# Kernel optimization log

Hardware: AMD Instinct MI355X
Metric: run time of the kernel (lower is better)

Reference implementation:

```python
import jax, jax.numpy as jnp
import numpy as np

N_NODES = 50000
N_EDGES = 800000
F_IN, F_HID, F_OUT = 128, 64, 32


def setup_inputs() -> dict:
    key = jax.random.key(0)
    k1, k2, k3, k4, k5, k6 = jax.random.split(key, 6)
    x = jax.random.normal(k1, (N_NODES, F_IN), dtype=jnp.float32)
    edge_index = jax.random.randint(k2, (2, N_EDGES), 0, N_NODES, dtype=jnp.int64)
    # Glorot-ish init for the two GCNConv linear layers
    W1 = jax.random.normal(k3, (F_IN, F_HID), dtype=jnp.float32) / np.sqrt(F_IN)
    b1 = jnp.zeros((F_HID,), dtype=jnp.float32)
    W2 = jax.random.normal(k4, (F_HID, F_OUT), dtype=jnp.float32) / np.sqrt(F_HID)
    b2 = jnp.zeros((F_OUT,), dtype=jnp.float32)
    return {"x": x, "edge_index": edge_index, "W1": W1, "b1": b1, "W2": W2, "b2": b2}


def _gcn_conv(x, src, dst, norm, W, b):
    # GCNConv: linear transform, then D^{-1/2}(A+I)D^{-1/2} aggregation
    xw = x @ W                                # [N, F_out]
    msg = xw[src] * norm[:, None]             # [E+N, F_out] gather + scale
    out = jax.ops.segment_sum(msg, dst, num_segments=x.shape[0])
    return out + b


def reference(x, edge_index, W1, b1, W2, b2):
    n = x.shape[0]
    self_loops = jnp.arange(n, dtype=edge_index.dtype)
    src = jnp.concatenate([edge_index[0], self_loops])  # [E+N]
    dst = jnp.concatenate([edge_index[1], self_loops])
    # symmetric degree normalization (self-loops guarantee deg >= 1)
    deg = jax.ops.segment_sum(jnp.ones_like(dst, dtype=x.dtype), dst, num_segments=n)
    dinv = jax.lax.rsqrt(deg)
    norm = dinv[src] * dinv[dst]              # [E+N]

    h = _gcn_conv(x, src, dst, norm, W1, b1)
    h = jax.nn.relu(h)
    # dropout p=0.5 is identity in eval mode (training=False)
    out = _gcn_conv(h, src, dst, norm, W2, b2)
    return out
```

## Files before the change

kernel.cpp:

```cpp
#include <hip/hip_runtime.h>
#include <hip/hip_fp16.h>

#define NN 50000
#define NE 800000
#define F_IN 128
#define F_HID 64
#define F_OUT 32
#define CAP 48
#define NBUCK 196
#define EPB 4096
#define CELL 64
#define NXW1 782

typedef _Float16 f16x8 __attribute__((ext_vector_type(8)));
typedef float f32x4 __attribute__((ext_vector_type(4)));
#define XS_STR 136


__global__ __launch_bounds__(256) void fused_xw1_partition_kernel(
        const float* __restrict__ x, const float* __restrict__ W,
        const int* __restrict__ src, const int* __restrict__ dst,
        int* __restrict__ cnt2t, unsigned int* __restrict__ bstore2,
        __half* __restrict__ outh) {
    __shared__ _Float16 xs[64 * XS_STR];
    __shared__ _Float16 wt[64 * XS_STR];
    __shared__ int hist[4][NBUCK];
    __shared__ int cur[NBUCK];
    int t = threadIdx.x;

    if (blockIdx.x < NBUCK) {
        int blk = blockIdx.x;
        for (int i = t; i < 4 * NBUCK; i += 256) ((int*)hist)[i] = 0;
        __syncthreads();
        int wv = t >> 6;
        int base = blk * EPB;
        unsigned int pk[16];
#pragma unroll
        for (int i = 0; i < 16; ++i) {
            int e = base + i * 256 + t;
            if (e < NE) {
                unsigned int d = (unsigned int)dst[e];
                unsigned int s = (unsigned int)src[e];
                pk[i] = (d << 16) | s;
                atomicAdd(&hist[wv][d >> 8], 1);
            } else {
                pk[i] = 0xFFFFFFFFu;
            }
        }
        __syncthreads();
        for (int b = t; b < NBUCK; b += 256) {
            int h = hist[0][b] + hist[1][b] + hist[2][b] + hist[3][b];
            cur[b] = 0;
            cnt2t[b * NBUCK + blk] = h;
        }
        __syncthreads();
#pragma unroll
        for (int i = 0; i < 16; ++i) {
            unsigned int p = pk[i];
            if (p != 0xFFFFFFFFu) {
                int b = p >> 24;
                int pos = atomicAdd(&cur[b], 1);
                if (pos < CELL) bstore2[((size_t)blk * NBUCK + b) * CELL + pos] = p;
            }
        }
        return;
    }

    int node0 = (blockIdx.x - NBUCK) * 64;

    {
        int r = t >> 2;
        int c0 = (t & 3) * 32;
        int gn = node0 + r;
        if (gn > NN - 1) gn = NN - 1;
        const float4* xrow = (const float4*)(x + (size_t)gn * F_IN);
#pragma unroll
        for (int i = 0; i < 8; ++i) {
            float4 v = xrow[(c0 >> 2) + i];
            _Float16* p = &xs[r * XS_STR + c0 + i * 4];
            p[0] = (_Float16)v.x; p[1] = (_Float16)v.y;
            p[2] = (_Float16)v.z; p[3] = (_Float16)v.w;
        }
    }
#pragma unroll
    for (int i = 0; i < 8; ++i) {
        int idx4 = t + i * 256;
        int k = idx4 >> 4;
        int n0 = (idx4 & 15) << 2;
        float4 v = ((const float4*)W)[idx4];
        wt[(n0 + 0) * XS_STR + k] = (_Float16)v.x;
        wt[(n0 + 1) * XS_STR + k] = (_Float16)v.y;
        wt[(n0 + 2) * XS_STR + k] = (_Float16)v.z;
        wt[(n0 + 3) * XS_STR + k] = (_Float16)v.w;
    }
    __syncthreads();

    int wave = t >> 6;
    int l = t & 63;
    int quad = l >> 4;
    int lm = l & 15;

    f32x4 acc[4] = {{0,0,0,0},{0,0,0,0},{0,0,0,0},{0,0,0,0}};
    const _Float16* abase = &xs[(wave * 16 + lm) * XS_STR + quad * 8];
#pragma unroll
    for (int kk4 = 0; kk4 < 4; ++kk4) {
        int kk = kk4 * 32;
        f16x8 a = *(const f16x8*)(abase + kk);
#pragma unroll
        for (int ft = 0; ft < 4; ++ft) {
            f16x8 b = *(const f16x8*)&wt[(ft * 16 + lm) * XS_STR + kk + quad * 8];
            acc[ft] = __builtin_amdgcn_mfma_f32_16x16x32_f16(a, b, acc[ft], 0, 0, 0);
        }
    }

    __syncthreads();
    _Float16* ot = xs;
#pragma unroll
    for (int ft = 0; ft < 4; ++ft) {
#pragma unroll
        for (int r = 0; r < 4; ++r) {
            int row_l = wave * 16 + quad * 4 + r;
            ot[row_l * 64 + ft * 16 + lm] = (_Float16)acc[ft][r];
        }
    }
    __syncthreads();
#pragma unroll
    for (int i = 0; i < 2; ++i) {
        int idx = t + i * 256;
        int row = idx >> 3;
        int c8 = (idx & 7) * 8;
        int gn = node0 + row;
        if (gn < NN)
            *(uint4*)(outh + (size_t)gn * 64 + c8) = *(const uint4*)&ot[row * 64 + c8];
    }
}


__device__ __forceinline__ void slot_insert(unsigned int p, int* cnt_l,
                                            unsigned short* slot_l) {
    int dl = (p >> 16) & 255;
    int pos = atomicAdd(&cnt_l[dl], 1);
    if (pos < CAP) slot_l[dl * CAP + pos] = (unsigned short)(p & 0xFFFFu);
}

__global__ __launch_bounds__(256) void build_slots_kernel(
        const int* __restrict__ cnt2t, const unsigned int* __restrict__ bstore2,
        unsigned short* __restrict__ slot, int* __restrict__ cnt_g, float* __restrict__ dinv) {
    __shared__ unsigned short slot_l[256 * CAP];
    __shared__ int cnt_l[256];
    int t = threadIdx.x;
    int b = blockIdx.x;
    cnt_l[t] = 0;
    __syncthreads();

    for (int blk = t; blk < NBUCK; blk += 256) {
        int c = cnt2t[b * NBUCK + blk];
        if (c > CELL) c = CELL;
        const unsigned int* seg = bstore2 + ((size_t)blk * NBUCK + b) * CELL;
        int j = 0;
        for (; j + 4 <= c; j += 4) {
            unsigned int p0 = seg[j + 0];
            unsigned int p1 = seg[j + 1];
            unsigned int p2 = seg[j + 2];
            unsigned int p3 = seg[j + 3];
            slot_insert(p0, cnt_l, slot_l);
            slot_insert(p1, cnt_l, slot_l);
            slot_insert(p2, cnt_l, slot_l);
            slot_insert(p3, cnt_l, slot_l);
        }
        for (; j < c; ++j) slot_insert(seg[j], cnt_l, slot_l);
    }
    __syncthreads();

    unsigned int* sg = (unsigned int*)(slot + (size_t)b * 256 * CAP);
    const unsigned int* sl = (const unsigned int*)slot_l;
    for (int j = t; j < 256 * CAP / 2; j += 256) sg[j] = sl[j];

    int n = b * 256 + t;
    if (n < NN) {
        int c = cnt_l[t];
        cnt_g[n] = c;
        dinv[n] = rsqrtf(1.0f + (float)c);
    }
}


__global__ __launch_bounds__(256, 4) void gather64_w2_kernel(
        const __half* __restrict__ xw, const int* __restrict__ cnt,
        const unsigned short* __restrict__ slot, const float* __restrict__ dinv,
        const float* __restrict__ b1, const float* __restrict__ W2,
        __half* __restrict__ hw2h) {
    __shared__ float w2s[F_HID * F_OUT];
    __shared__ float hl[4][F_HID];
    int t = threadIdx.x;
    for (int i = t; i < F_HID * F_OUT / 4; i += 256)
        ((float4*)w2s)[i] = ((const float4*)W2)[i];
    __syncthreads();

    int lane = t & 63;
    int wv = t >> 6;
    int n = blockIdx.x * 4 + wv;
    int st = lane >> 4;
    int fl4 = lane & 15;
    const uint2* base = (const uint2*)xw;
    int deg = cnt[n];
    if (deg > CAP) deg = CAP;
    float din = dinv[n];
    const unsigned short* srow = slot + (size_t)n * CAP;
    float a0 = 0, a1 = 0, a2 = 0, a3 = 0;
    int e = st;
    for (; e + 12 < deg; e += 16) {
        int s0 = srow[e];
        int s1 = srow[e + 4];
        int s2 = srow[e + 8];
        int s3 = srow[e + 12];
        float dv0 = dinv[s0], dv1 = dinv[s1], dv2 = dinv[s2], dv3 = dinv[s3];
        uint2 u0 = base[(size_t)s0 * 16 + fl4];
        uint2 u1 = base[(size_t)s1 * 16 + fl4];
        uint2 u2 = base[(size_t)s2 * 16 + fl4];
        uint2 u3 = base[(size_t)s3 * 16 + fl4];
        float2 p0 = __half22float2(*(__half2*)&u0.x), p1 = __half22float2(*(__half2*)&u0.y);
        float2 q0 = __half22float2(*(__half2*)&u1.x), q1 = __half22float2(*(__half2*)&u1.y);
        float2 r0 = __half22float2(*(__half2*)&u2.x), r1 = __half22float2(*(__half2*)&u2.y);
        float2 t0 = __half22float2(*(__half2*)&u3.x), t1 = __half22float2(*(__half2*)&u3.y);
        a0 += dv0 * p0.x + dv1 * q0.x + dv2 * r0.x + dv3 * t0.x;
        a1 += dv0 * p0.y + dv1 * q0.y + dv2 * r0.y + dv3 * t0.y;
        a2 += dv0 * p1.x + dv1 * q1.x + dv2 * r1.x + dv3 * t1.x;
        a3 += dv0 * p1.y + dv1 * q1.y + dv2 * r1.y + dv3 * t1.y;
    }
    for (; e < deg; e += 4) {
        int s = srow[e];
        float dv = dinv[s];
        uint2 u = base[(size_t)s * 16 + fl4];
        float2 p0 = __half22float2(*(__half2*)&u.x);
        float2 p1 = __half22float2(*(__half2*)&u.y);
        a0 += dv * p0.x; a1 += dv * p0.y; a2 += dv * p1.x; a3 += dv * p1.y;
    }
    a0 += __shfl_xor(a0, 16, 64); a1 += __shfl_xor(a1, 16, 64);
    a2 += __shfl_xor(a2, 16, 64); a3 += __shfl_xor(a3, 16, 64);
    a0 += __shfl_xor(a0, 32, 64); a1 += __shfl_xor(a1, 32, 64);
    a2 += __shfl_xor(a2, 32, 64); a3 += __shfl_xor(a3, 32, 64);
    if (st == 0) {
        uint2 u = base[(size_t)n * 16 + fl4];
        float2 s0 = __half22float2(*(__half2*)&u.x);
        float2 s1 = __half22float2(*(__half2*)&u.y);
        float4 bb = ((const float4*)b1)[fl4];
        float v0 = din * (a0 + din * s0.x) + bb.x;
        float v1 = din * (a1 + din * s0.y) + bb.y;
        float v2 = din * (a2 + din * s1.x) + bb.z;
        float v3 = din * (a3 + din * s1.y) + bb.w;
        float* hr = &hl[wv][fl4 * 4];
        hr[0] = v0 > 0.f ? v0 : 0.f;
        hr[1] = v1 > 0.f ? v1 : 0.f;
        hr[2] = v2 > 0.f ? v2 : 0.f;
        hr[3] = v3 > 0.f ? v3 : 0.f;
    }
    asm volatile("s_waitcnt lgkmcnt(0)" ::: "memory");
    {
        int f = lane & 31;
        int kh = lane >> 5;
        const float* hr = &hl[wv][kh * 32];
        float acc = 0.0f;
#pragma unroll
        for (int k = 0; k < 32; ++k) acc += hr[k] * w2s[(kh * 32 + k) * F_OUT + f];
        acc += __shfl_xor(acc, 32, 64);
        if (kh == 0) hw2h[(size_t)n * F_OUT + f] = __float2half(acc * din);
    }
}


__global__ __launch_bounds__(256, 8) void gather32_kernel(
        const __half* __restrict__ scaled, const int* __restrict__ cnt,
        const unsigned short* __restrict__ slot, const float* __restrict__ dinv,
        const float* __restrict__ bias, float* __restrict__ out) {
    int lane = threadIdx.x & 63;
    int n = blockIdx.x * 4 + (threadIdx.x >> 6);
    if (n >= NN) return;
    int st = lane >> 3;
    int fl4 = lane & 7;
    const uint2* base = (const uint2*)scaled;
    int deg = cnt[n];
    if (deg > CAP) deg = CAP;
    const unsigned short* srow = slot + (size_t)n * CAP;
    float a0 = 0, a1 = 0, a2 = 0, a3 = 0;
    int e = st;
    for (; e + 8 < deg; e += 16) {
        int s0 = srow[e];
        int s1 = srow[e + 8];
        uint2 u0 = base[(size_t)s0 * 8 + fl4];
        uint2 u1 = base[(size_t)s1 * 8 + fl4];
        float2 p0 = __half22float2(*(__half2*)&u0.x);
        float2 p1 = __half22float2(*(__half2*)&u0.y);
        float2 q0 = __half22float2(*(__half2*)&u1.x);
        float2 q1 = __half22float2(*(__half2*)&u1.y);
        a0 += p0.x + q0.x; a1 += p0.y + q0.y;
        a2 += p1.x + q1.x; a3 += p1.y + q1.y;
    }
    for (; e < deg; e += 8) {
        int s = srow[e];
        uint2 u = base[(size_t)s * 8 + fl4];
        float2 p0 = __half22float2(*(__half2*)&u.x);
        float2 p1 = __half22float2(*(__half2*)&u.y);
        a0 += p0.x; a1 += p0.y; a2 += p1.x; a3 += p1.y;
    }
    a0 += __shfl_xor(a0, 8, 64);  a1 += __shfl_xor(a1, 8, 64);
    a2 += __shfl_xor(a2, 8, 64);  a3 += __shfl_xor(a3, 8, 64);
    a0 += __shfl_xor(a0, 16, 64); a1 += __shfl_xor(a1, 16, 64);
    a2 += __shfl_xor(a2, 16, 64); a3 += __shfl_xor(a3, 16, 64);
    a0 += __shfl_xor(a0, 32, 64); a1 += __shfl_xor(a1, 32, 64);
    a2 += __shfl_xor(a2, 32, 64); a3 += __shfl_xor(a3, 32, 64);
    if (st == 0) {
        uint2 u = base[(size_t)n * 8 + fl4];
        float2 s0 = __half22float2(*(__half2*)&u.x);
        float2 s1 = __half22float2(*(__half2*)&u.y);
        float4 b4 = ((const float4*)bias)[fl4];
        float di = dinv[n];
        float4 r;
        r.x = di * (a0 + s0.x) + b4.x;
        r.y = di * (a1 + s0.y) + b4.y;
        r.z = di * (a2 + s1.x) + b4.z;
        r.w = di * (a3 + s1.y) + b4.w;
        ((float4*)out)[(size_t)n * 8 + fl4] = r;
    }
}


extern "C" void kernel_launch(void* const* d_in, const int* in_sizes, int n_in,
                              void* d_out, int out_size, void* d_ws, size_t ws_size,
                              hipStream_t stream) {
    const float* x  = (const float*)d_in[0];
    const int*   ei = (const int*)d_in[1];
    const float* W1 = (const float*)d_in[2];
    const float* b1 = (const float*)d_in[3];
    const float* W2 = (const float*)d_in[4];
    const float* b2 = (const float*)d_in[5];
    const int* src = ei;
    const int* dst = ei + NE;

    float*          ws      = (float*)d_ws;
    float*          dinv    = ws;
    int*            cnt     = (int*)(ws + 50048);
    int*            cnt2t   = (int*)(ws + 100096);
    unsigned int*   bstore2 = (unsigned int*)(ws + 138624);
    unsigned short* slot    = (unsigned short*)(ws + 2597248);
    __half*         xw1h    = (__half*)(ws + 3801472);
    __half*         hw2h    = (__half*)(ws + 5401472);
    float*          out     = (float*)d_out;

    fused_xw1_partition_kernel<<<NBUCK + NXW1, 256, 0, stream>>>(
        x, W1, src, dst, cnt2t, bstore2, xw1h);
    build_slots_kernel<<<NBUCK, 256, 0, stream>>>(cnt2t, bstore2, slot, cnt, dinv);
    gather64_w2_kernel<<<NN / 4, 256, 0, stream>>>(xw1h, cnt, slot, dinv, b1, W2, hw2h);
    gather32_kernel<<<NN / 4, 256, 0, stream>>>(hw2h, cnt, slot, dinv, b2, out);
}
```

Measured before the change: 150.6 us.

## Merge four kernels into one persistent kernel with software grid barriers

Replaces the four separate launches (partition plus XW1, slot build, layer-1 gather with W2, layer-2 gather) with a single persistent kernel. It is sized to the occupancy-limited resident grid, loops over work units, and separates phases with atomic-counter grid barriers. The aim is to remove per-launch overhead and inter-kernel gaps. In exchange it adds system-scope fences and spin-waits at each barrier, a memset and host-side property queries on every call. The grid is also capped at 1024 blocks and limited by the shared union LDS, which may reduce parallelism in the gather phases.

Result: slower. 515.9 us (+242.6%).

```diff
diff --git a/kernel.cpp b/kernel.cpp
--- a/kernel.cpp
+++ b/kernel.cpp
@@ -11,316 +11,323 @@
 #define EPB 4096
 #define CELL 64
 #define NXW1 782
+#define NGRP 12500
 
 typedef _Float16 f16x8 __attribute__((ext_vector_type(8)));
 typedef float f32x4 __attribute__((ext_vector_type(4)));
 #define XS_STR 136
 
-
-__global__ __launch_bounds__(256) void fused_xw1_partition_kernel(
-        const float* __restrict__ x, const float* __restrict__ W,
+__device__ __forceinline__ void grid_barrier(int* bar, int phase, int G) {
+    __syncthreads();
+    if (threadIdx.x == 0) {
+        __threadfence_system();
+        int ticket = __hip_atomic_fetch_add(&bar[0], 1, __ATOMIC_ACQ_REL,
+                                            __HIP_MEMORY_SCOPE_SYSTEM);
+        if (ticket == phase * G - 1) {
+            __threadfence_system();
+            __hip_atomic_store(&bar[1], phase, __ATOMIC_RELEASE,
+                               __HIP_MEMORY_SCOPE_SYSTEM);
+        } else {
+            while (__hip_atomic_load(&bar[1], __ATOMIC_ACQUIRE,
+                                     __HIP_MEMORY_SCOPE_SYSTEM) < phase)
+                __builtin_amdgcn_s_sleep(8);
+        }
+        __threadfence_system();
+    }
+    __syncthreads();
+}
+
+__global__ __launch_bounds__(256, 4) void mega_kernel(
+        const float* __restrict__ x, const float* __restrict__ W1,
+        const float* __restrict__ b1, const float* __restrict__ W2,
+        const float* __restrict__ b2,
         const int* __restrict__ src, const int* __restrict__ dst,
         int* __restrict__ cnt2t, unsigned int* __restrict__ bstore2,
-        __half* __restrict__ outh) {
-    __shared__ _Float16 xs[64 * XS_STR];
-    __shared__ _Float16 wt[64 * XS_STR];
-    __shared__ int hist[4][NBUCK];
-    __shared__ int cur[NBUCK];
+        unsigned short* __restrict__ slot, int* __restrict__ cnt_g,
+        float* __restrict__ dinv, __half* __restrict__ xw1h,
+        __half* __restrict__ hw2h, float* __restrict__ out, int* bar) {
+    __shared__ __align__(16) char lds[34816];
     int t = threadIdx.x;
-
-    if (blockIdx.x < NBUCK) {
-        int blk = blockIdx.x;
-        for (int i = t; i < 4 * NBUCK; i += 256) ((int*)hist)[i] = 0;
-        __syncthreads();
+    int G = gridDim.x;
+
+    for (int u = blockIdx.x; u < NBUCK + NXW1; u += G) {
+        __syncthreads();
+        if (u < NBUCK) {
+            int blk = u;
+            int (*hist)[NBUCK] = (int(*)[NBUCK])lds;
+            int* cur = (int*)(lds + 3136);
+            for (int i = t; i < 4 * NBUCK; i += 256) ((int*)hist)[i] = 0;
+            __syncthreads();
+            int wv = t >> 6;
+            int base = blk * EPB;
+            unsigned int pk[16];
+#pragma unroll
+            for (int i = 0; i < 16; ++i) {
+                int e = base + i * 256 + t;
+                if (e < NE) {
+                    unsigned int d = (unsigned int)dst[e];
+                    unsigned int s = (unsigned int)src[e];
+                    pk[i] = (d << 16) | s;
+                    atomicAdd(&hist[wv][d >> 8], 1);
+                } else pk[i] = 0xFFFFFFFFu;
+            }
+            __syncthreads();
+            for (int b = t; b < NBUCK; b += 256) {
+                cur[b] = 0;
+                cnt2t[b * NBUCK + blk] = hist[0][b] + hist[1][b] + hist[2][b] + hist[3][b];
+            }
+            __syncthreads();
+#pragma unroll
+            for (int i = 0; i < 16; ++i) {
+                unsigned int p = pk[i];
+                if (p != 0xFFFFFFFFu) {
+                    int b = p >> 24;
+                    int pos = atomicAdd(&cur[b], 1);
+                    if (pos < CELL) bstore2[((size_t)blk * NBUCK + b) * CELL + pos] = p;
+                }
+            }
+        } else {
+            int node0 = (u - NBUCK) * 64;
+            _Float16* xs = (_Float16*)lds;
+            _Float16* wt = xs + 64 * XS_STR;
+            {
+                int r = t >> 2;
+                int c0 = (t & 3) * 32;
+                int gn = node0 + r;
+                if (gn > NN - 1) gn = NN - 1;
+                const float4* xrow = (const float4*)(x + (size_t)gn * F_IN);
+#pragma unroll
+                for (int i = 0; i < 8; ++i) {
+                    float4 v = xrow[(c0 >> 2) + i];
+                    _Float16* p = &xs[r * XS_STR + c0 + i * 4];
+                    p[0] = (_Float16)v.x; p[1] = (_Float16)v.y;
+                    p[2] = (_Float16)v.z; p[3] = (_Float16)v.w;
+                }
+            }
+#pragma unroll
+            for (int i = 0; i < 8; ++i) {
+                int idx4 = t + i * 256;
+                int k = idx4 >> 4;
+                int n0 = (idx4 & 15) << 2;
+                float4 v = ((const float4*)W1)[idx4];
+                wt[(n0 + 0) * XS_STR + k] = (_Float16)v.x;
+                wt[(n0 + 1) * XS_STR + k] = (_Float16)v.y;
+                wt[(n0 + 2) * XS_STR + k] = (_Float16)v.z;
+                wt[(n0 + 3) * XS_STR + k] = (_Float16)v.w;
+            }
+            __syncthreads();
+            int wave = t >> 6;
+            int l = t & 63;
+            int quad = l >> 4;
+            int lm = l & 15;
+            f32x4 acc[4] = {{0,0,0,0},{0,0,0,0},{0,0,0,0},{0,0,0,0}};
+            const _Float16* abase = &xs[(wave * 16 + lm) * XS_STR + quad * 8];
+#pragma unroll
+            for (int kk4 = 0; kk4 < 4; ++kk4) {
+                int kk = kk4 * 32;
+                f16x8 a = *(const f16x8*)(abase + kk);
+#pragma unroll
+                for (int ft = 0; ft < 4; ++ft) {
+                    f16x8 b = *(const f16x8*)&wt[(ft * 16 + lm) * XS_STR + kk + quad * 8];
+                    acc[ft] = __builtin_amdgcn_mfma_f32_16x16x32_f16(a, b, acc[ft], 0, 0, 0);
+                }
+            }
+            __syncthreads();
+            _Float16* ot = xs;
+#pragma unroll
+            for (int ft = 0; ft < 4; ++ft) {
+#pragma unroll
+                for (int r = 0; r < 4; ++r) {
+                    int row_l = wave * 16 + quad * 4 + r;
+                    ot[row_l * 64 + ft * 16 + lm] = (_Float16)acc[ft][r];
+                }
+            }
+            __syncthreads();
+#pragma unroll
+            for (int i = 0; i < 2; ++i) {
+                int idx = t + i * 256;
+                int row = idx >> 3;
+                int c8 = (idx & 7) * 8;
+                int gn = node0 + row;
+                if (gn < NN)
+                    *(uint4*)(xw1h + (size_t)gn * 64 + c8) = *(const uint4*)&ot[row * 64 + c8];
+            }
+        }
+    }
+    grid_barrier(bar, 1, G);
+
+    for (int b = blockIdx.x; b < NBUCK; b += G) {
+        unsigned short* slot_l = (unsigned short*)lds;
+        int* cnt_l = (int*)(lds + 24576);
+        cnt_l[t] = 0;
+        __syncthreads();
+        for (int blk = t; blk < NBUCK; blk += 256) {
+            int c = cnt2t[b * NBUCK + blk];
+            if (c > CELL) c = CELL;
+            const unsigned int* seg = bstore2 + ((size_t)blk * NBUCK + b) * CELL;
+            int j = 0;
+            for (; j + 4 <= c; j += 4) {
+                unsigned int p0 = seg[j + 0];
+                unsigned int p1 = seg[j + 1];
+                unsigned int p2 = seg[j + 2];
+                unsigned int p3 = seg[j + 3];
+#pragma unroll
+                for (int q = 0; q < 4; ++q) {
+                    unsigned int p = (q == 0) ? p0 : (q == 1) ? p1 : (q == 2) ? p2 : p3;
+                    int dl = (p >> 16) & 255;
+                    int pos = atomicAdd(&cnt_l[dl], 1);
+                    if (pos < CAP) slot_l[dl * CAP + pos] = (unsigned short)(p & 0xFFFFu);
+                }
+            }
+            for (; j < c; ++j) {
+                unsigned int p = seg[j];
+                int dl = (p >> 16) & 255;
+                int pos = atomicAdd(&cnt_l[dl], 1);
+                if (pos < CAP) slot_l[dl * CAP + pos] = (unsigned short)(p & 0xFFFFu);
+            }
+        }
+        __syncthreads();
+        unsigned int* sg = (unsigned int*)(slot + (size_t)b * 256 * CAP);
+        const unsigned int* sl = (const unsigned int*)slot_l;
+        for (int j = t; j < 256 * CAP / 2; j += 256) sg[j] = sl[j];
+        int n = b * 256 + t;
+        if (n < NN) {
+            int c = cnt_l[t];
+            cnt_g[n] = c;
+            dinv[n] = rsqrtf(1.0f + (float)c);
+        }
+        __syncthreads();
+    }
+    grid_barrier(bar, 2, G);
+
+    {
+        float* w2s = (float*)lds;
+        float (*hl)[F_HID] = (float(*)[F_HID])(lds + 8192);
+        for (int i = t; i < F_HID * F_OUT / 4; i += 256)
+            ((float4*)w2s)[i] = ((const float4*)W2)[i];
+        __syncthreads();
+        int lane = t & 63;
         int wv = t >> 6;
-        int base = blk * EPB;
-        unsigned int pk[16];
-#pragma unroll
-        for (int i = 0; i < 16; ++i) {
-            int e = base + i * 256 + t;
-            if (e < NE) {
-                unsigned int d = (unsigned int)dst[e];
-                unsigned int s = (unsigned int)src[e];
-                pk[i] = (d << 16) | s;
-                atomicAdd(&hist[wv][d >> 8], 1);
-            } else {
-                pk[i] = 0xFFFFFFFFu;
-            }
-        }
-        __syncthreads();
-        for (int b = t; b < NBUCK; b += 256) {
-            int h = hist[0][b] + hist[1][b] + hist[2][b] + hist[3][b];
-            cur[b] = 0;
-            cnt2t[b * NBUCK + blk] = h;
-        }
-        __syncthreads();
-#pragma unroll
-        for (int i = 0; i < 16; ++i) {
-            unsigned int p = pk[i];
-            if (p != 0xFFFFFFFFu) {
-                int b = p >> 24;
-                int pos = atomicAdd(&cur[b], 1);
-                if (pos < CELL) bstore2[((size_t)blk * NBUCK + b) * CELL + pos] = p;
-            }
-        }
-        return;
-    }
-
-    int node0 = (blockIdx.x - NBUCK) * 64;
+        int st = lane >> 4;
+        int fl4 = lane & 15;
+        const uint2* base = (const uint2*)xw1h;
+        for (int g = blockIdx.x; g < NGRP; g += G) {
+            int n = g * 4 + wv;
+            int deg = cnt_g[n];
+            if (deg > CAP) deg = CAP;
+            float din = dinv[n];
+            const unsigned short* srow = slot + (size_t)n * CAP;
+            float a0 = 0, a1 = 0, a2 = 0, a3 = 0;
+            int e = st;
+            for (; e + 12 < deg; e += 16) {
+                int s0 = srow[e], s1 = srow[e + 4], s2 = srow[e + 8], s3 = srow[e + 12];
+                float dv0 = dinv[s0], dv1 = dinv[s1], dv2 = dinv[s2], dv3 = dinv[s3];
+                uint2 u0 = base[(size_t)s0 * 16 + fl4];
+                uint2 u1 = base[(size_t)s1 * 16 + fl4];
+                uint2 u2 = base[(size_t)s2 * 16 + fl4];
+                uint2 u3 = base[(size_t)s3 * 16 + fl4];
+                float2 p0 = __half22float2(*(__half2*)&u0.x), p1 = __half22float2(*(__half2*)&u0.y);
+                float2 q0 = __half22float2(*(__half2*)&u1.x), q1 = __half22float2(*(__half2*)&u1.y);
+                float2 r0 = __half22float2(*(__half2*)&u2.x), r1 = __half22float2(*(__half2*)&u2.y);
+                float2 t0 = __half22float2(*(__half2*)&u3.x), t1 = __half22float2(*(__half2*)&u3.y);
+                a0 += dv0 * p0.x + dv1 * q0.x + dv2 * r0.x + dv3 * t0.x;
+                a1 += dv0 * p0.y + dv1 * q0.y + dv2 * r0.y + dv3 * t0.y;
+                a2 += dv0 * p1.x + dv1 * q1.x + dv2 * r1.x + dv3 * t1.x;
+                a3 += dv0 * p1.y + dv1 * q1.y + dv2 * r1.y + dv3 * t1.y;
+            }
+            for (; e < deg; e += 4) {
+                int s = srow[e];
+                float dv = dinv[s];
+                uint2 u = base[(size_t)s * 16 + fl4];
+                float2 p0 = __half22float2(*(__half2*)&u.x);
+                float2 p1 = __half22float2(*(__half2*)&u.y);
+                a0 += dv * p0.x; a1 += dv * p0.y; a2 += dv * p1.x; a3 += dv * p1.y;
+            }
+            a0 += __shfl_xor(a0, 16, 64); a1 += __shfl_xor(a1, 16, 64);
+            a2 += __shfl_xor(a2, 16, 64); a3 += __shfl_xor(a3, 16, 64);
+            a0 += __shfl_xor(a0, 32, 64); a1 += __shfl_xor(a1, 32, 64);
+            a2 += __shfl_xor(a2, 32, 64); a3 += __shfl_xor(a3, 32, 64);
+            if (st == 0) {
+                uint2 u = base[(size_t)n * 16 + fl4];
+                float2 s0 = __half22float2(*(__half2*)&u.x);
+                float2 s1 = __half22float2(*(__half2*)&u.y);
+                float4 bb = ((const float4*)b1)[fl4];
+                float v0 = din * (a0 + din * s0.x) + bb.x;
+                float v1 = din * (a1 + din * s0.y) + bb.y;
+                float v2 = din * (a2 + din * s1.x) + bb.z;
+                float v3 = din * (a3 + din * s1.y) + bb.w;
+                float* hr = &hl[wv][fl4 * 4];
+                hr[0] = v0 > 0.f ? v0 : 0.f;
+                hr[1] = v1 > 0.f ? v1 : 0.f;
+                hr[2] = v2 > 0.f ? v2 : 0.f;
+                hr[3] = v3 > 0.f ? v3 : 0.f;
+            }
+            asm volatile("s_waitcnt lgkmcnt(0)" ::: "memory");
+            {
+                int f = lane & 31;
+                int kh = lane >> 5;
+                const float* hr = &hl[wv][kh * 32];
+                float acc = 0.0f;
+#pragma unroll
+                for (int k = 0; k < 32; ++k) acc += hr[k] * w2s[(kh * 32 + k) * F_OUT + f];
+                acc += __shfl_xor(acc, 32, 64);
+                if (kh == 0) hw2h[(size_t)n * F_OUT + f] = __float2half(acc * din);
+            }
+        }
+    }
+    grid_barrier(bar, 3, G);
 
     {
-        int r = t >> 2;
-        int c0 = (t & 3) * 32;
-        int gn = node0 + r;
-        if (gn > NN - 1) gn = NN - 1;
-        const float4* xrow = (const float4*)(x + (size_t)gn * F_IN);
-#pragma unroll
-        for (int i = 0; i < 8; ++i) {
-            float4 v = xrow[(c0 >> 2) + i];
-            _Float16* p = &xs[r * XS_STR + c0 + i * 4];
-            p[0] = (_Float16)v.x; p[1] = (_Float16)v.y;
-            p[2] = (_Float16)v.z; p[3] = (_Float16)v.w;
-        }
-    }
-#pragma unroll
-    for (int i = 0; i < 8; ++i) {
-        int idx4 = t + i * 256;
-        int k = idx4 >> 4;
-        int n0 = (idx4 & 15) << 2;
-        float4 v = ((const float4*)W)[idx4];
-        wt[(n0 + 0) * XS_STR + k] = (_Float16)v.x;
-        wt[(n0 + 1) * XS_STR + k] = (_Float16)v.y;
-        wt[(n0 + 2) * XS_STR + k] = (_Float16)v.z;
-        wt[(n0 + 3) * XS_STR + k] = (_Float16)v.w;
-    }
-    __syncthreads();
-
-    int wave = t >> 6;
-    int l = t & 63;
-    int quad = l >> 4;
-    int lm = l & 15;
-
-    f32x4 acc[4] = {{0,0,0,0},{0,0,0,0},{0,0,0,0},{0,0,0,0}};
-    const _Float16* abase = &xs[(wave * 16 + lm) * XS_STR + quad * 8];
-#pragma unroll
-    for (int kk4 = 0; kk4 < 4; ++kk4) {
-        int kk = kk4 * 32;
-        f16x8 a = *(const f16x8*)(abase + kk);
-#pragma unroll
-        for (int ft = 0; ft < 4; ++ft) {
-            f16x8 b = *(const f16x8*)&wt[(ft * 16 + lm) * XS_STR + kk + quad * 8];
-            acc[ft] = __builtin_amdgcn_mfma_f32_16x16x32_f16(a, b, acc[ft], 0, 0, 0);
-        }
-    }
-
-    __syncthreads();
-    _Float16* ot = xs;
-#pragma unroll
-    for (int ft = 0; ft < 4; ++ft) {
-#pragma unroll
-        for (int r = 0; r < 4; ++r) {
-            int row_l = wave * 16 + quad * 4 + r;
-            ot[row_l * 64 + ft * 16 + lm] = (_Float16)acc[ft][r];
-        }
-    }
-    __syncthreads();
-#pragma unroll
-    for (int i = 0; i < 2; ++i) {
-        int idx = t + i * 256;
-        int row = idx >> 3;
-        int c8 = (idx & 7) * 8;
-        int gn = node0 + row;
-        if (gn < NN)
-            *(uint4*)(outh + (size_t)gn * 64 + c8) = *(const uint4*)&ot[row * 64 + c8];
-    }
-}
-
-
-__device__ __forceinline__ void slot_insert(unsigned int p, int* cnt_l,
-                                            unsigned short* slot_l) {
-    int dl = (p >> 16) & 255;
-    int pos = atomicAdd(&cnt_l[dl], 1);
-    if (pos < CAP) slot_l[dl * CAP + pos] = (unsigned short)(p & 0xFFFFu);
-}
-
-__global__ __launch_bounds__(256) void build_slots_kernel(
-        const int* __restrict__ cnt2t, const unsigned int* __restrict__ bstore2,
-        unsigned short* __restrict__ slot, int* __restrict__ cnt_g, float* __restrict__ dinv) {
-    __shared__ unsigned short slot_l[256 * CAP];
-    __shared__ int cnt_l[256];
-    int t = threadIdx.x;
-    int b = blockIdx.x;
-    cnt_l[t] = 0;
-    __syncthreads();
-
-    for (int blk = t; blk < NBUCK; blk += 256) {
-        int c = cnt2t[b * NBUCK + blk];
-        if (c > CELL) c = CELL;
-        const unsigned int* seg = bstore2 + ((size_t)blk * NBUCK + b) * CELL;
-        int j = 0;
-        for (; j + 4 <= c; j += 4) {
-            unsigned int p0 = seg[j + 0];
-            unsigned int p1 = seg[j + 1];
-            unsigned int p2 = seg[j + 2];
-            unsigned int p3 = seg[j + 3];
-            slot_insert(p0, cnt_l, slot_l);
-            slot_insert(p1, cnt_l, slot_l);
-            slot_insert(p2, cnt_l, slot_l);
-            slot_insert(p3, cnt_l, slot_l);
-        }
-        for (; j < c; ++j) slot_insert(seg[j], cnt_l, slot_l);
-    }
-    __syncthreads();
-
-    unsigned int* sg = (unsigned int*)(slot + (size_t)b * 256 * CAP);
-    const unsigned int* sl = (const unsigned int*)slot_l;
-    for (int j = t; j < 256 * CAP / 2; j += 256) sg[j] = sl[j];
-
-    int n = b * 256 + t;
-    if (n < NN) {
-        int c = cnt_l[t];
-        cnt_g[n] = c;
-        dinv[n] = rsqrtf(1.0f + (float)c);
-    }
-}
-
-
-__global__ __launch_bounds__(256, 4) void gather64_w2_kernel(
-        const __half* __restrict__ xw, const int* __restrict__ cnt,
-        const unsigned short* __restrict__ slot, const float* __restrict__ dinv,
-        const float* __restrict__ b1, const float* __restrict__ W2,
-        __half* __restrict__ hw2h) {
-    __shared__ float w2s[F_HID * F_OUT];
-    __shared__ float hl[4][F_HID];
-    int t = threadIdx.x;
-    for (int i = t; i < F_HID * F_OUT / 4; i += 256)
-        ((float4*)w2s)[i] = ((const float4*)W2)[i];
-    __syncthreads();
-
-    int lane = t & 63;
-    int wv = t >> 6;
-    int n = blockIdx.x * 4 + wv;
-    int st = lane >> 4;
-    int fl4 = lane & 15;
-    const uint2* base = (const uint2*)xw;
-    int deg = cnt[n];
-    if (deg > CAP) deg = CAP;
-    float din = dinv[n];
-    const unsigned short* srow = slot + (size_t)n * CAP;
-    float a0 = 0, a1 = 0, a2 = 0, a3 = 0;
-    int e = st;
-    for (; e + 12 < deg; e += 16) {
-        int s0 = srow[e];
-        int s1 = srow[e + 4];
-        int s2 = srow[e + 8];
-        int s3 = srow[e + 12];
-        float dv0 = dinv[s0], dv1 = dinv[s1], dv2 = dinv[s2], dv3 = dinv[s3];
-        uint2 u0 = base[(size_t)s0 * 16 + fl4];
-        uint2 u1 = base[(size_t)s1 * 16 + fl4];
-        uint2 u2 = base[(size_t)s2 * 16 + fl4];
-        uint2 u3 = base[(size_t)s3 * 16 + fl4];
-        float2 p0 = __half22float2(*(__half2*)&u0.x), p1 = __half22float2(*(__half2*)&u0.y);
-        float2 q0 = __half22float2(*(__half2*)&u1.x), q1 = __half22float2(*(__half2*)&u1.y);
-        float2 r0 = __half22float2(*(__half2*)&u2.x), r1 = __half22float2(*(__half2*)&u2.y);
-        float2 t0 = __half22float2(*(__half2*)&u3.x), t1 = __half22float2(*(__half2*)&u3.y);
-        a0 += dv0 * p0.x + dv1 * q0.x + dv2 * r0.x + dv3 * t0.x;
-        a1 += dv0 * p0.y + dv1 * q0.y + dv2 * r0.y + dv3 * t0.y;
-        a2 += dv0 * p1.x + dv1 * q1.x + dv2 * r1.x + dv3 * t1.x;
-        a3 += dv0 * p1.y + dv1 * q1.y + dv2 * r1.y + dv3 * t1.y;
-    }
-    for (; e < deg; e += 4) {
-        int s = srow[e];
-        float dv = dinv[s];
-        uint2 u = base[(size_t)s * 16 + fl4];
-        float2 p0 = __half22float2(*(__half2*)&u.x);
-        float2 p1 = __half22float2(*(__half2*)&u.y);
-        a0 += dv * p0.x; a1 += dv * p0.y; a2 += dv * p1.x; a3 += dv * p1.y;
-    }
-    a0 += __shfl_xor(a0, 16, 64); a1 += __shfl_xor(a1, 16, 64);
-    a2 += __shfl_xor(a2, 16, 64); a3 += __shfl_xor(a3, 16, 64);
-    a0 += __shfl_xor(a0, 32, 64); a1 += __shfl_xor(a1, 32, 64);
-    a2 += __shfl_xor(a2, 32, 64); a3 += __shfl_xor(a3, 32, 64);
-    if (st == 0) {
-        uint2 u = base[(size_t)n * 16 + fl4];
-        float2 s0 = __half22float2(*(__half2*)&u.x);
-        float2 s1 = __half22float2(*(__half2*)&u.y);
-        float4 bb = ((const float4*)b1)[fl4];
-        float v0 = din * (a0 + din * s0.x) + bb.x;
-        float v1 = din * (a1 + din * s0.y) + bb.y;
-        float v2 = din * (a2 + din * s1.x) + bb.z;
-        float v3 = din * (a3 + din * s1.y) + bb.w;
-        float* hr = &hl[wv][fl4 * 4];
-        hr[0] = v0 > 0.f ? v0 : 0.f;
-        hr[1] = v1 > 0.f ? v1 : 0.f;
-        hr[2] = v2 > 0.f ? v2 : 0.f;
-        hr[3] = v3 > 0.f ? v3 : 0.f;
-    }
-    asm volatile("s_waitcnt lgkmcnt(0)" ::: "memory");
-    {
-        int f = lane & 31;
-        int kh = lane >> 5;
-        const float* hr = &hl[wv][kh * 32];
-        float acc = 0.0f;
-#pragma unroll
-        for (int k = 0; k < 32; ++k) acc += hr[k] * w2s[(kh * 32 + k) * F_OUT + f];
-        acc += __shfl_xor(acc, 32, 64);
-        if (kh == 0) hw2h[(size_t)n * F_OUT + f] = __float2half(acc * din);
-    }
-}
-
-
-__global__ __launch_bounds__(256, 8) void gather32_kernel(
-        const __half* __restrict__ scaled, const int* __restrict__ cnt,
-        const unsigned short* __restrict__ slot, const float* __restrict__ dinv,
-        const float* __restrict__ bias, float* __restrict__ out) {
-    int lane = threadIdx.x & 63;
-    int n = blockIdx.x * 4 + (threadIdx.x >> 6);
-    if (n >= NN) return;
-    int st = lane >> 3;
-    int fl4 = lane & 7;
-    const uint2* base = (const uint2*)scaled;
-    int deg = cnt[n];
-    if (deg > CAP) deg = CAP;
-    const unsigned short* srow = slot + (size_t)n * CAP;
-    float a0 = 0, a1 = 0, a2 = 0, a3 = 0;
-    int e = st;
-    for (; e + 8 < deg; e += 16) {
-        int s0 = srow[e];
-        int s1 = srow[e + 8];
-        uint2 u0 = base[(size_t)s0 * 8 + fl4];
-        uint2 u1 = base[(size_t)s1 * 8 + fl4];
-        float2 p0 = __half22float2(*(__half2*)&u0.x);
-        float2 p1 = __half22float2(*(__half2*)&u0.y);
-        float2 q0 = __half22float2(*(__half2*)&u1.x);
-        float2 q1 = __half22float2(*(__half2*)&u1.y);
-        a0 += p0.x + q0.x; a1 += p0.y + q0.y;
-        a2 += p1.x + q1.x; a3 += p1.y + q1.y;
-    }
-    for (; e < deg; e += 8) {
-        int s = srow[e];
-        uint2 u = base[(size_t)s * 8 + fl4];
-        float2 p0 = __half22float2(*(__half2*)&u.x);
-        float2 p1 = __half22float2(*(__half2*)&u.y);
-        a0 += p0.x; a1 += p0.y; a2 += p1.x; a3 += p1.y;
-    }
-    a0 += __shfl_xor(a0, 8, 64);  a1 += __shfl_xor(a1, 8, 64);
-    a2 += __shfl_xor(a2, 8, 64);  a3 += __shfl_xor(a3, 8, 64);
-    a0 += __shfl_xor(a0, 16, 64); a1 += __shfl_xor(a1, 16, 64);
-    a2 += __shfl_xor(a2, 16, 64); a3 += __shfl_xor(a3, 16, 64);
-    a0 += __shfl_xor(a0, 32, 64); a1 += __shfl_xor(a1, 32, 64);
-    a2 += __shfl_xor(a2, 32, 64); a3 += __shfl_xor(a3, 32, 64);
-    if (st == 0) {
-        uint2 u = base[(size_t)n * 8 + fl4];
-        float2 s0 = __half22float2(*(__half2*)&u.x);
-        float2 s1 = __half22float2(*(__half2*)&u.y);
-        float4 b4 = ((const float4*)bias)[fl4];
-        float di = dinv[n];
-        float4 r;
-        r.x = di * (a0 + s0.x) + b4.x;
-        r.y = di * (a1 + s0.y) + b4.y;
-        r.z = di * (a2 + s1.x) + b4.z;
-        r.w = di * (a3 + s1.y) + b4.w;
-        ((float4*)out)[(size_t)n * 8 + fl4] = r;
+        int lane = t & 63;
+        int wv = t >> 6;
+        int st = lane >> 3;
+        int fl4 = lane & 7;
+        const uint2* base = (const uint2*)hw2h;
+        for (int g = blockIdx.x; g < NGRP; g += G) {
+            int n = g * 4 + wv;
+            int deg = cnt_g[n];
+            if (deg > CAP) deg = CAP;
+            const unsigned short* srow = slot + (size_t)n * CAP;
+            float a0 = 0, a1 = 0, a2 = 0, a3 = 0;
+            int e = st;
+            for (; e + 8 < deg; e += 16) {
+                int s0 = srow[e], s1 = srow[e + 8];
+                uint2 u0 = base[(size_t)s0 * 8 + fl4];
+                uint2 u1 = base[(size_t)s1 * 8 + fl4];
+                float2 p0 = __half22float2(*(__half2*)&u0.x);
+                float2 p1 = __half22float2(*(__half2*)&u0.y);
+                float2 q0 = __half22float2(*(__half2*)&u1.x);
+                float2 q1 = __half22float2(*(__half2*)&u1.y);
+                a0 += p0.x + q0.x; a1 += p0.y + q0.y;
+                a2 += p1.x + q1.x; a3 += p1.y + q1.y;
+            }
+            for (; e < deg; e += 8) {
+                int s = srow[e];
+                uint2 u = base[(size_t)s * 8 + fl4];
+                float2 p0 = __half22float2(*(__half2*)&u.x);
+                float2 p1 = __half22float2(*(__half2*)&u.y);
+                a0 += p0.x; a1 += p0.y; a2 += p1.x; a3 += p1.y;
+            }
+            a0 += __shfl_xor(a0, 8, 64);  a1 += __shfl_xor(a1, 8, 64);
+            a2 += __shfl_xor(a2, 8, 64);  a3 += __shfl_xor(a3, 8, 64);
+            a0 += __shfl_xor(a0, 16, 64); a1 += __shfl_xor(a1, 16, 64);
+            a2 += __shfl_xor(a2, 16, 64); a3 += __shfl_xor(a3, 16, 64);
+            a0 += __shfl_xor(a0, 32, 64); a1 += __shfl_xor(a1, 32, 64);
+            a2 += __shfl_xor(a2, 32, 64); a3 += __shfl_xor(a3, 32, 64);
+            if (st == 0) {
+                uint2 u = base[(size_t)n * 8 + fl4];
+                float2 s0 = __half22float2(*(__half2*)&u.x);
+                float2 s1 = __half22float2(*(__half2*)&u.y);
+                float4 b4 = ((const float4*)b2)[fl4];
+                float di = dinv[n];
+                float4 r;
+                r.x = di * (a0 + s0.x) + b4.x;
+                r.y = di * (a1 + s0.y) + b4.y;
+                r.z = di * (a2 + s1.x) + b4.z;
+                r.w = di * (a3 + s1.y) + b4.w;
+                ((float4*)out)[(size_t)n * 8 + fl4] = r;
+            }
+        }
     }
 }
 
@@ -345,11 +352,21 @@
     unsigned short* slot    = (unsigned short*)(ws + 2597248);
     __half*         xw1h    = (__half*)(ws + 3801472);
     __half*         hw2h    = (__half*)(ws + 5401472);
+    int*            bar     = (int*)(ws + 6201472);
     float*          out     = (float*)d_out;
 
-    fused_xw1_partition_kernel<<<NBUCK + NXW1, 256, 0, stream>>>(
-        x, W1, src, dst, cnt2t, bstore2, xw1h);
-    build_slots_kernel<<<NBUCK, 256, 0, stream>>>(cnt2t, bstore2, slot, cnt, dinv);
-    gather64_w2_kernel<<<NN / 4, 256, 0, stream>>>(xw1h, cnt, slot, dinv, b1, W2, hw2h);
-    gather32_kernel<<<NN / 4, 256, 0, stream>>>(hw2h, cnt, slot, dinv, b2, out);
+    int perCU = 0;
+    hipOccupancyMaxActiveBlocksPerMultiprocessor(&perCU, mega_kernel, 256, 0);
+    if (perCU < 1) perCU = 1;
+    int dev = 0;
+    hipGetDevice(&dev);
+    hipDeviceProp_t prop;
+    hipGetDeviceProperties(&prop, dev);
+    int grid = perCU * prop.multiProcessorCount;
+    if (grid > 1024) grid = 1024;
+
+    hipMemsetAsync(bar, 0, 2 * sizeof(int), stream);
+    mega_kernel<<<grid, 256, 0, stream>>>(
+        x, W1, b1, W2, b2, src, dst,
+        cnt2t, bstore2, slot, cnt, dinv, xw1h, hw2h, out, bar);
 }
```
